# Kernel optimization log

Measured on AMD Instinct MI355X. Metric: run time of the kernel, lower is better.

## Reference

```python
import jax, jax.numpy as jnp
import numpy as np

B, L, H = 16, 4096, 256

def setup_inputs() -> dict:
    key = jax.random.key(0)
    k1, k2, k3 = jax.random.split(key, 3)
    scale = 1.0 / np.sqrt(H)
    x = jax.random.normal(k1, (B, L, H), dtype=jnp.float32)
    Wv = jax.random.normal(k2, (H, H), dtype=jnp.float32) * scale  # value_proj weight (torch Linear: y = x @ W.T)
    Wo = jax.random.normal(k3, (H, H), dtype=jnp.float32) * scale  # out_proj weight
    return {"x": x, "Wv": Wv, "Wo": Wo}

def reference(x, Wv, Wo):
    # x: [B, L, H]
    Bx, Lx, Hx = x.shape
    # Causal uniform-average 'attention' matrix: T[i, j] = 1/(i+1) for j <= i, else 0.
    tril = jnp.tril(jnp.ones((Lx, Lx), dtype=x.dtype))
    counts = jnp.arange(1, Lx + 1, dtype=x.dtype)[:, None]  # row-wise counts = i+1
    T = tril / counts
    # v = out_proj(value_proj(x)); torch Linear applies W.T on the right
    v = (x @ Wv.T) @ Wo.T                       # [B, L, H]
    # mixed[b, i] = mean over j <= i of v[b, j]  (== causal cumulative mean)
    mixed = jnp.einsum('ij,bjh->bih', T, v)     # [B, L, H]
    # dropout is identity in eval mode; pre_ln residual
    return x + mixed
```

## Files before the change

kernel.cpp:

```cpp
#include <hip/hip_runtime.h>
#include <hip/hip_bf16.h>


#define B_  16
#define L_  4096
#define H_  256
#define M_  (B_*L_)
#define K_  256
#define CH  64
#define CHROWS (L_/CH)

typedef short short8 __attribute__((ext_vector_type(8)));
typedef float f32x4  __attribute__((ext_vector_type(4)));

__device__ __forceinline__ unsigned short f2bf(float f) {
  unsigned int u = __builtin_bit_cast(unsigned int, f);
  u += 0x7fffu + ((u >> 16) & 1u);
  return (unsigned short)(u >> 16);
}

__device__ __forceinline__ void gload_lds16(const void* g, void* l) {
  __builtin_amdgcn_global_load_lds(
      (const __attribute__((address_space(1))) unsigned int*)g,
      (__attribute__((address_space(3))) unsigned int*)l,
      16, 0, 0);
}

__global__ void fuse_w_kernel(const float* __restrict__ Wv,
                              const float* __restrict__ Wo,
                              unsigned short* __restrict__ Wbf) {
  __shared__ float wo[H_];
  int h = blockIdx.x, t = threadIdx.x;
  wo[t] = Wo[h*H_ + t];
  __syncthreads();
  float acc = 0.f;
  #pragma unroll 8
  for (int m = 0; m < H_; ++m) acc += wo[m] * Wv[m*H_ + t];
  Wbf[h*H_ + t] = f2bf(acc);
}

__global__ void partial_kernel(const float* __restrict__ x, float* __restrict__ P) {
  int c = blockIdx.x, b = blockIdx.y, t = threadIdx.x;
  const float* p = x + ((size_t)(b*L_ + c*CHROWS))*H_ + t;
  float s = 0.f;
  #pragma unroll 8
  for (int r = 0; r < CHROWS; ++r) s += p[(size_t)r*H_];
  P[(b*CH + c)*H_ + t] = s;
}

__global__ void scan_kernel(const float* __restrict__ P, float* __restrict__ O) {
  int b = blockIdx.x, t = threadIdx.x;
  float run = 0.f;
  for (int c = 0; c < CH; ++c) {
    int idx = (b*CH + c)*H_ + t;
    O[idx] = run;
    run += P[idx];
  }
}

__global__ void cumsum_kernel(const float* __restrict__ x, const float* __restrict__ O,
                              unsigned short* __restrict__ Sbf) {
  int c = blockIdx.x, b = blockIdx.y, t = threadIdx.x;
  size_t base = ((size_t)(b*L_ + c*CHROWS))*H_ + t;
  float run = O[(b*CH + c)*H_ + t];
  for (int r = 0; r < CHROWS; ++r) {
    run += x[base + (size_t)r*H_];
    Sbf[base + (size_t)r*H_] = f2bf(run);
  }
}

#define BM 128
#define BN 128
#define BK 64

__global__ __launch_bounds__(256, 2) void gemm_kernel(
    const unsigned short* __restrict__ Sbf,
    const unsigned short* __restrict__ Wbf,
    const float* __restrict__ x,
    float* __restrict__ out) {
  __shared__ __align__(16) unsigned short As[BM*BK];
  __shared__ __align__(16) unsigned short Bs[BN*BK];
  const int tid = threadIdx.x;
  const int rowBase = blockIdx.x * BM;
  const int colBase = blockIdx.y * BN;
  const int wave = tid >> 6, lane = tid & 63;
  const int wr = wave >> 1, wc = wave & 1;
  const int lrow = lane & 15;
  const int lk   = lane >> 4;

  f32x4 acc[4][4] = {};

  for (int t = 0; t < K_/BK; ++t) {
    const int k0 = t * BK;
    #pragma unroll
    for (int it = 0; it < 4; ++it) {
      int off = it*4096 + tid*16;
      int r = off >> 7, cb = off & 127;
      gload_lds16((const char*)Sbf + ((size_t)(rowBase + r))*512 + k0*2 + cb,
                  (char*)As + off);
      gload_lds16((const char*)Wbf + ((size_t)(colBase + r))*512 + k0*2 + cb,
                  (char*)Bs + off);
    }
    __syncthreads();
    #pragma unroll
    for (int ks = 0; ks < 2; ++ks) {
      short8 a[4], b[4];
      #pragma unroll
      for (int i = 0; i < 4; ++i) {
        int ar = wr*64 + i*16 + lrow;
        a[i] = *(const short8*)((const char*)As + ar*128 + ks*64 + lk*16);
        int br = wc*64 + i*16 + lrow;
        b[i] = *(const short8*)((const char*)Bs + br*128 + ks*64 + lk*16);
      }
      #pragma unroll
      for (int i = 0; i < 4; ++i)
        #pragma unroll
        for (int j = 0; j < 4; ++j)
          acc[i][j] = __builtin_amdgcn_mfma_f32_16x16x32_bf16(a[i], b[j], acc[i][j], 0, 0, 0);
    }
    __syncthreads();
  }

  #pragma unroll
  for (int i = 0; i < 4; ++i) {
    #pragma unroll
    for (int j4 = 0; j4 < 4; ++j4) {
      int row = rowBase + wr*64 + i*16 + lk*4 + j4;
      float scale = 1.0f / (float)((row & (L_-1)) + 1);
      size_t rb = (size_t)row * H_;
      #pragma unroll
      for (int n = 0; n < 4; ++n) {
        int col = colBase + wc*64 + n*16 + lrow;
        out[rb + col] = x[rb + col] + acc[i][n][j4] * scale;
      }
    }
  }
}

extern "C" void kernel_launch(void* const* d_in, const int* in_sizes, int n_in,
                              void* d_out, int out_size, void* d_ws, size_t ws_size,
                              hipStream_t stream) {
  const float* x  = (const float*)d_in[0];
  const float* Wv = (const float*)d_in[1];
  const float* Wo = (const float*)d_in[2];
  float* out = (float*)d_out;

  char* ws = (char*)d_ws;
  unsigned short* Sbf = (unsigned short*)ws;
  unsigned short* Wbf = (unsigned short*)(ws + (size_t)M_*K_*2);
  float* P = (float*)(ws + (size_t)M_*K_*2 + (size_t)H_*H_*2);
  float* O = P + B_*CH*H_;

  hipLaunchKernelGGL(fuse_w_kernel,  dim3(H_),      dim3(H_), 0, stream, Wv, Wo, Wbf);
  hipLaunchKernelGGL(partial_kernel, dim3(CH, B_),  dim3(H_), 0, stream, x, P);
  hipLaunchKernelGGL(scan_kernel,    dim3(B_),      dim3(H_), 0, stream, P, O);
  hipLaunchKernelGGL(cumsum_kernel,  dim3(CH, B_),  dim3(H_), 0, stream, x, O, Sbf);
  hipLaunchKernelGGL(gemm_kernel,    dim3(M_/BM, H_/BN), dim3(256), 0, stream,
                     Sbf, Wbf, x, out);
}
```

Measured before the change: 76.32 us.

## Fuse in-chunk cumsum into GEMM and drop the bf16 prefix-sum buffer

```diff
diff --git a/kernel.cpp b/kernel.cpp
--- a/kernel.cpp
+++ b/kernel.cpp
@@ -6,9 +6,8 @@
 #define L_  4096
 #define H_  256
 #define M_  (B_*L_)
-#define K_  256
 #define CH  64
-#define CHROWS (L_/CH)
+#define CHROWS 64
 
 typedef short short8 __attribute__((ext_vector_type(8)));
 typedef float f32x4  __attribute__((ext_vector_type(4)));
@@ -17,13 +16,6 @@
   unsigned int u = __builtin_bit_cast(unsigned int, f);
   u += 0x7fffu + ((u >> 16) & 1u);
   return (unsigned short)(u >> 16);
-}
-
-__device__ __forceinline__ void gload_lds16(const void* g, void* l) {
-  __builtin_amdgcn_global_load_lds(
-      (const __attribute__((address_space(1))) unsigned int*)g,
-      (__attribute__((address_space(3))) unsigned int*)l,
-      16, 0, 0);
 }
 
 __global__ void fuse_w_kernel(const float* __restrict__ Wv,
@@ -51,6 +43,7 @@
 __global__ void scan_kernel(const float* __restrict__ P, float* __restrict__ O) {
   int b = blockIdx.x, t = threadIdx.x;
   float run = 0.f;
+  #pragma unroll
   for (int c = 0; c < CH; ++c) {
     int idx = (b*CH + c)*H_ + t;
     O[idx] = run;
@@ -58,67 +51,63 @@
   }
 }
 
-__global__ void cumsum_kernel(const float* __restrict__ x, const float* __restrict__ O,
-                              unsigned short* __restrict__ Sbf) {
-  int c = blockIdx.x, b = blockIdx.y, t = threadIdx.x;
-  size_t base = ((size_t)(b*L_ + c*CHROWS))*H_ + t;
-  float run = O[(b*CH + c)*H_ + t];
-  for (int r = 0; r < CHROWS; ++r) {
-    run += x[base + (size_t)r*H_];
-    Sbf[base + (size_t)r*H_] = f2bf(run);
-  }
-}
+#define BM 128
 
-#define BM 128
-#define BN 128
-#define BK 64
+__global__ __launch_bounds__(512, 2) void gemm_fused(
+    const float* __restrict__ x,
+    const unsigned short* __restrict__ Wbf,
+    const float* __restrict__ O,
+    float* __restrict__ out) {
+  __shared__ __align__(16) unsigned short As[BM * H_];
+  char* Asb = (char*)As;
 
-__global__ __launch_bounds__(256, 2) void gemm_kernel(
-    const unsigned short* __restrict__ Sbf,
-    const unsigned short* __restrict__ Wbf,
-    const float* __restrict__ x,
-    float* __restrict__ out) {
-  __shared__ __align__(16) unsigned short As[BM*BK];
-  __shared__ __align__(16) unsigned short Bs[BN*BK];
   const int tid = threadIdx.x;
   const int rowBase = blockIdx.x * BM;
-  const int colBase = blockIdx.y * BN;
+  const int b  = rowBase >> 12;
+  const int ri = rowBase & (L_ - 1);
+
+  if (tid < H_) {
+    const int t = tid;
+    float run = O[((b << 6) + (ri >> 6)) * H_ + t];
+    const float* xp = x + (size_t)rowBase * H_ + t;
+    #pragma unroll 8
+    for (int r = 0; r < BM; ++r) {
+      run += xp[(size_t)r * H_];
+      int pc = (2*t) ^ ((r & 7) << 4);
+      *(unsigned short*)(Asb + r*512 + pc) = f2bf(run);
+    }
+  }
+  __syncthreads();
+
   const int wave = tid >> 6, lane = tid & 63;
-  const int wr = wave >> 1, wc = wave & 1;
+  const int wr = wave >> 2, wc = wave & 3;
   const int lrow = lane & 15;
   const int lk   = lane >> 4;
 
   f32x4 acc[4][4] = {};
 
-  for (int t = 0; t < K_/BK; ++t) {
-    const int k0 = t * BK;
-    #pragma unroll
-    for (int it = 0; it < 4; ++it) {
-      int off = it*4096 + tid*16;
-      int r = off >> 7, cb = off & 127;
-      gload_lds16((const char*)Sbf + ((size_t)(rowBase + r))*512 + k0*2 + cb,
-                  (char*)As + off);
-      gload_lds16((const char*)Wbf + ((size_t)(colBase + r))*512 + k0*2 + cb,
-                  (char*)Bs + off);
-    }
-    __syncthreads();
+  for (int k0 = 0; k0 < H_; k0 += 64) {
     #pragma unroll
     for (int ks = 0; ks < 2; ++ks) {
-      short8 a[4], b[4];
+      short8 bf[4];
+      #pragma unroll
+      for (int n = 0; n < 4; ++n) {
+        int wrow = wc*64 + n*16 + lrow;
+        bf[n] = *(const short8*)(Wbf + (size_t)wrow*H_ + k0 + ks*32 + lk*8);
+      }
+      short8 af[4];
       #pragma unroll
       for (int i = 0; i < 4; ++i) {
         int ar = wr*64 + i*16 + lrow;
-        a[i] = *(const short8*)((const char*)As + ar*128 + ks*64 + lk*16);
-        int br = wc*64 + i*16 + lrow;
-        b[i] = *(const short8*)((const char*)Bs + br*128 + ks*64 + lk*16);
+        int cb = (k0*2 + ks*64 + lk*16) ^ ((ar & 7) << 4);
+        af[i] = *(const short8*)(Asb + ar*512 + cb);
       }
       #pragma unroll
       for (int i = 0; i < 4; ++i)
         #pragma unroll
-        for (int j = 0; j < 4; ++j)
-          acc[i][j] = __builtin_amdgcn_mfma_f32_16x16x32_bf16(a[i], b[j], acc[i][j], 0, 0, 0);
+        for (int n = 0; n < 4; ++n)
+          acc[i][n] = __builtin_amdgcn_mfma_f32_16x16x32_bf16(af[i], bf[n], acc[i][n], 0, 0, 0);
     }
-    __syncthreads();
   }
 
   #pragma unroll
@@ -126,11 +115,11 @@
     #pragma unroll
     for (int j4 = 0; j4 < 4; ++j4) {
       int row = rowBase + wr*64 + i*16 + lk*4 + j4;
-      float scale = 1.0f / (float)((row & (L_-1)) + 1);
+      float scale = 1.0f / (float)((row & (L_ - 1)) + 1);
       size_t rb = (size_t)row * H_;
       #pragma unroll
       for (int n = 0; n < 4; ++n) {
-        int col = colBase + wc*64 + n*16 + lrow;
+        int col = wc*64 + n*16 + lrow;
         out[rb + col] = x[rb + col] + acc[i][n][j4] * scale;
       }
     }
@@ -146,15 +135,13 @@
   float* out = (float*)d_out;
 
   char* ws = (char*)d_ws;
-  unsigned short* Sbf = (unsigned short*)ws;
-  unsigned short* Wbf = (unsigned short*)(ws + (size_t)M_*K_*2);
-  float* P = (float*)(ws + (size_t)M_*K_*2 + (size_t)H_*H_*2);
-  float* O = P + B_*CH*H_;
+  unsigned short* Wbf = (unsigned short*)ws;
+  float* P = (float*)(ws + (size_t)H_*H_*2);
+  float* Off = P + B_*CH*H_;
 
-  hipLaunchKernelGGL(fuse_w_kernel,  dim3(H_),      dim3(H_), 0, stream, Wv, Wo, Wbf);
-  hipLaunchKernelGGL(partial_kernel, dim3(CH, B_),  dim3(H_), 0, stream, x, P);
-  hipLaunchKernelGGL(scan_kernel,    dim3(B_),      dim3(H_), 0, stream, P, O);
-  hipLaunchKernelGGL(cumsum_kernel,  dim3(CH, B_),  dim3(H_), 0, stream, x, O, Sbf);
-  hipLaunchKernelGGL(gemm_kernel,    dim3(M_/BM, H_/BN), dim3(256), 0, stream,
-                     Sbf, Wbf, x, out);
+  hipLaunchKernelGGL(fuse_w_kernel,  dim3(H_),     dim3(H_), 0, stream, Wv, Wo, Wbf);
+  hipLaunchKernelGGL(partial_kernel, dim3(CH, B_), dim3(H_), 0, stream, x, P);
+  hipLaunchKernelGGL(scan_kernel,    dim3(B_),     dim3(H_), 0, stream, P, Off);
+  hipLaunchKernelGGL(gemm_fused,     dim3(M_/BM),  dim3(512), 0, stream,
+                     x, Wbf, Off, out);
 }
```

Result: slower. 90.86 us (+19.0%).
